# Kernel tuning notes

Measured on AMD Instinct MI355X. Metric: run time of the kernel, lower is better.

The kernel has to match this reference:

```python
import jax, jax.numpy as jnp
import numpy as np

B, S, D = 1, 2048, 2048
H, HKV, HD = 16, 8, 128
WINDOW = 1024
EPS = 1e-6
SCALE = HD ** -0.5


def _rope_tables(seq_len, head_dim, theta=10000.0):
    inv_freq = 1.0 / (theta ** (jnp.arange(0, head_dim, 2, dtype=jnp.float32) / head_dim))
    ang = jnp.arange(seq_len, dtype=jnp.float32)[:, None] * inv_freq[None, :]  # [S, hd/2]
    emb = jnp.concatenate([ang, ang], axis=-1)  # [S, hd]
    return jnp.cos(emb)[None], jnp.sin(emb)[None]  # [1, S, hd]


def setup_inputs() -> dict:
    key = jax.random.key(0)
    ks = jax.random.split(key, 8)
    cos, sin = _rope_tables(S, HD)
    return {
        "hidden_states": jax.random.normal(ks[0], (B, S, D), jnp.float32),
        "cos": jnp.broadcast_to(cos, (B, S, HD)),
        "sin": jnp.broadcast_to(sin, (B, S, HD)),
        "Wq": jax.random.normal(ks[1], (D, H * HD), jnp.float32) * (D ** -0.5),
        "Wk": jax.random.normal(ks[2], (D, HKV * HD), jnp.float32) * (D ** -0.5),
        "Wv": jax.random.normal(ks[3], (D, HKV * HD), jnp.float32) * (D ** -0.5),
        "Wo": jax.random.normal(ks[4], (H * HD, D), jnp.float32) * ((H * HD) ** -0.5),
        "q_scale": jax.random.uniform(ks[5], (HD,), jnp.float32, 0.5, 1.5),
        "k_scale": jax.random.uniform(ks[6], (HD,), jnp.float32, 0.5, 1.5),
    }


def _rms_norm(x, scale):
    # per-head RMSNorm over last dim, computed in fp32 (matches RMSNorm module)
    xf = x.astype(jnp.float32)
    var = jnp.mean(xf * xf, axis=-1, keepdims=True)
    return (xf * jax.lax.rsqrt(var + EPS) * scale).astype(x.dtype)


def _rotate_half(x):
    x1, x2 = x[..., : HD // 2], x[..., HD // 2 :]
    return jnp.concatenate([-x2, x1], axis=-1)


def _apply_rope(x, cos, sin):
    # cos/sin: [B,S,hd] -> [B,S,1,hd] (unsqueeze_dim=2)
    c, s = cos[:, :, None, :], sin[:, :, None, :]
    return x * c + _rotate_half(x) * s


def reference(hidden_states, cos, sin, Wq, Wk, Wv, Wo, q_scale, k_scale):
    b, s, _ = hidden_states.shape
    q = (hidden_states @ Wq).reshape(b, s, H, HD)
    k = (hidden_states @ Wk).reshape(b, s, HKV, HD)
    v = (hidden_states @ Wv).reshape(b, s, HKV, HD)
    q = _rms_norm(q, q_scale)
    k = _rms_norm(k, k_scale)
    q = _apply_rope(q, cos, sin)
    k = _apply_rope(k, cos, sin)
    # GQA: repeat kv heads to match query heads (groups are consecutive)
    g = H // HKV
    k = jnp.repeat(k, g, axis=2)  # [b, s, H, hd]
    v = jnp.repeat(v, g, axis=2)
    scores = jnp.einsum("bqhd,bkhd->bhqk", q, k) * SCALE  # [b,H,S,S]
    i = jnp.arange(s)[:, None]
    j = jnp.arange(s)[None, :]
    allowed = (j <= i) & (i - j <= WINDOW)  # causal + sliding window
    scores = jnp.where(allowed[None, None], scores, -jnp.inf)
    attn = jax.nn.softmax(scores, axis=-1)
    out = jnp.einsum("bhqk,bkhd->bqhd", attn, v).reshape(b, s, H * HD)
    return out @ Wo
```

## Files before the change

kernel.cpp:

```cpp
#include <hip/hip_runtime.h>
#include <hip/hip_bf16.h>
#include <cmath>


typedef __bf16 bf16x8 __attribute__((ext_vector_type(8)));
typedef float  f32x4  __attribute__((ext_vector_type(4)));

#define S_LEN    2048
#define NH       16
#define NKV      8
#define HDIM     128
#define WIN      1024
#define QK_SCALE_L2E 0.12751744595f
#define RMS_EPS  1e-6f

__device__ __forceinline__ void gld16(void* lds, const void* g) {
    __builtin_amdgcn_global_load_lds(
        (const __attribute__((address_space(1))) unsigned int*)g,
        (__attribute__((address_space(3))) unsigned int*)lds, 16, 0, 0);
}

__device__ __forceinline__ unsigned short f2bu(float x) {
    __hip_bfloat16 h = __float2bfloat16(x);
    return *(unsigned short*)&h;
}

__global__ __launch_bounds__(256) void trans_cvt_kernel(
    const float* __restrict__ Wq, const float* __restrict__ Wk,
    const float* __restrict__ Wv, const float* __restrict__ Wo,
    const float* __restrict__ hs,
    __hip_bfloat16* __restrict__ WqkvT, __hip_bfloat16* __restrict__ WoT,
    __hip_bfloat16* __restrict__ hsb)
{
    __shared__ __attribute__((aligned(16))) unsigned short tile[64][72];
    int id = blockIdx.x;
    if (id >= 3072) {
        size_t i = ((size_t)(id - 3072) * 256 + threadIdx.x) * 8;
        float4 a = *(const float4*)(hs + i);
        float4 b = *(const float4*)(hs + i + 4);
        unsigned short u[8] = { f2bu(a.x), f2bu(a.y), f2bu(a.z), f2bu(a.w),
                                f2bu(b.x), f2bu(b.y), f2bu(b.z), f2bu(b.w) };
        *(uint4*)(hsb + i) = *(uint4*)u;
        return;
    }
    const float* src; __hip_bfloat16* dst; int N, kt, nt;
    if (id < 1024)      { src = Wq; dst = WqkvT;                          N = 2048; kt = id >> 5;          nt = id & 31; }
    else if (id < 1536) { src = Wk; dst = WqkvT + (size_t)2048*2048;      N = 1024; kt = (id-1024) >> 4;   nt = (id-1024) & 15; }
    else if (id < 2048) { src = Wv; dst = WqkvT + (size_t)3072*2048;      N = 1024; kt = (id-1536) >> 4;   nt = (id-1536) & 15; }
    else                { src = Wo; dst = WoT;                            N = 2048; kt = (id-2048) >> 5;   nt = (id-2048) & 31; }
    int k0 = kt * 64, n0 = nt * 64;
    int tid = threadIdx.x;
#pragma unroll
    for (int p = 0; p < 2; ++p) {
        int c = p*256 + tid; int r = c >> 3, cc = (c & 7) * 8;
        const float* s = src + (size_t)(k0 + r)*N + n0 + cc;
        float4 a = *(const float4*)s;
        float4 b = *(const float4*)(s + 4);
        unsigned short u[8] = { f2bu(a.x), f2bu(a.y), f2bu(a.z), f2bu(a.w),
                                f2bu(b.x), f2bu(b.y), f2bu(b.z), f2bu(b.w) };
        *(uint4*)&tile[r][cc] = *(uint4*)u;
    }
    __syncthreads();
#pragma unroll
    for (int p = 0; p < 2; ++p) {
        int c = p*256 + tid; int r2 = c >> 3, c2 = (c & 7) * 8;
        uint4 o;
        o.x = tile[c2+0][r2] | ((unsigned)tile[c2+1][r2] << 16);
        o.y = tile[c2+2][r2] | ((unsigned)tile[c2+3][r2] << 16);
        o.z = tile[c2+4][r2] | ((unsigned)tile[c2+5][r2] << 16);
        o.w = tile[c2+6][r2] | ((unsigned)tile[c2+7][r2] << 16);
        *(uint4*)(dst + (size_t)(n0 + r2)*2048 + k0 + c2) = o;
    }
}

template <typename OT>
__global__ __launch_bounds__(256) void gemm_bt_kernel(
    const __hip_bfloat16* __restrict__ A, const __hip_bfloat16* __restrict__ BT,
    OT* __restrict__ C, int M, int N, int K)
{
    __shared__ __attribute__((aligned(16))) __hip_bfloat16 As[128*32];
    __shared__ __attribute__((aligned(16))) __hip_bfloat16 Bs[128*32];
    const int tid  = threadIdx.x;
    const int lane = tid & 63;
    const int wave = tid >> 6;
    const int quad = lane >> 4, l15 = lane & 15;
    const int m0 = blockIdx.y * 128, n0 = blockIdx.x * 128;
    const int wm = (wave >> 1) * 64, wn = (wave & 1) * 64;
    const int sw = (quad ^ ((l15 >> 1) & 3)) * 8;

    f32x4 acc[4][4] = {};

    for (int k0 = 0; k0 < K; k0 += 32) {
#pragma unroll
        for (int p = 0; p < 2; ++p) {
            int c = p*256 + tid;
            int row = c >> 2, seg = c & 3;
            int cs = seg ^ ((row >> 1) & 3);
            gld16((char*)As + c*16, A  + (size_t)(m0 + row)*K + k0 + cs*8);
            gld16((char*)Bs + c*16, BT + (size_t)(n0 + row)*K + k0 + cs*8);
        }
        __syncthreads();
        bf16x8 af[4], bfr[4];
#pragma unroll
        for (int t = 0; t < 4; ++t) {
            af[t]  = *(const bf16x8*)(As + (wm + t*16 + l15)*32 + sw);
            bfr[t] = *(const bf16x8*)(Bs + (wn + t*16 + l15)*32 + sw);
        }
#pragma unroll
        for (int mt = 0; mt < 4; ++mt)
#pragma unroll
            for (int nt = 0; nt < 4; ++nt)
                acc[mt][nt] = __builtin_amdgcn_mfma_f32_16x16x32_bf16(af[mt], bfr[nt], acc[mt][nt], 0, 0, 0);
        __syncthreads();
    }
#pragma unroll
    for (int mt = 0; mt < 4; ++mt)
#pragma unroll
        for (int nt = 0; nt < 4; ++nt)
#pragma unroll
            for (int r = 0; r < 4; ++r) {
                int row = m0 + wm + mt*16 + quad*4 + r;
                int col = n0 + wn + nt*16 + l15;
                if constexpr (__is_same(OT, float))
                    C[(size_t)row*N + col] = acc[mt][nt][r];
                else
                    C[(size_t)row*N + col] = __float2bfloat16(acc[mt][nt][r]);
            }
}

__global__ __launch_bounds__(256) void rms_vt_kernel(
    const __hip_bfloat16* __restrict__ qkv,
    const float* __restrict__ cosb, const float* __restrict__ sinb,
    const float* __restrict__ qsc,  const float* __restrict__ ksc,
    __hip_bfloat16* __restrict__ Qn, __hip_bfloat16* __restrict__ Kn,
    __hip_bfloat16* __restrict__ Vt)
{
    __shared__ __attribute__((aligned(16))) unsigned short tile[64][72];
    int id = blockIdx.x;
    if (id >= 2048) {
        int t  = id - 2048;
        int s0 = (t & 31) * 64;
        int v0 = (t >> 5) * 64;
        int tid = threadIdx.x;
#pragma unroll
        for (int p = 0; p < 2; ++p) {
            int c = p*256 + tid; int r = c >> 3, cc = (c & 7) * 8;
            uint4 v = *(const uint4*)(qkv + (size_t)(s0 + r)*4096 + 3072 + v0 + cc);
            *(uint4*)&tile[r][cc] = v;
        }
        __syncthreads();
#pragma unroll
        for (int p = 0; p < 2; ++p) {
            int c = p*256 + tid; int r2 = c >> 3, c2 = (c & 7) * 8;
            uint4 o;
            o.x = tile[c2+0][r2] | ((unsigned)tile[c2+1][r2] << 16);
            o.y = tile[c2+2][r2] | ((unsigned)tile[c2+3][r2] << 16);
            o.z = tile[c2+4][r2] | ((unsigned)tile[c2+5][r2] << 16);
            o.w = tile[c2+6][r2] | ((unsigned)tile[c2+7][r2] << 16);
            *(uint4*)(Vt + (size_t)(v0 + r2)*2048 + s0 + c2) = o;
        }
        return;
    }
    int s = id;
    int wave = threadIdx.x >> 6, lane = threadIdx.x & 63;
    float c1 = cosb[s*128 + lane];
    float c2 = cosb[s*128 + 64 + lane];
    float s1 = sinb[s*128 + lane];
    float s2 = sinb[s*128 + 64 + lane];
    for (int u = wave; u < 24; u += 4) {
        bool isq = (u < 16);
        int h = isq ? u : u - 16;
        const __hip_bfloat16* x = qkv + (size_t)s*4096 + (isq ? h*128 : 2048 + h*128);
        float x1 = (float)x[lane], x2 = (float)x[lane + 64];
        float ss = x1*x1 + x2*x2;
#pragma unroll
        for (int off = 32; off; off >>= 1) ss += __shfl_xor(ss, off);
        float r = rsqrtf(ss * (1.0f/128.0f) + RMS_EPS);
        if (isq) r *= QK_SCALE_L2E;
        const float* sc = isq ? qsc : ksc;
        float y1 = x1 * r * sc[lane];
        float y2 = x2 * r * sc[lane + 64];
        float o1 = y1*c1 - y2*s1;
        float o2 = y2*c2 + y1*s2;
        __hip_bfloat16* dst = isq ? (Qn + (size_t)s*2048 + h*128)
                                  : (Kn + (size_t)s*1024 + h*128);
        dst[lane]      = __float2bfloat16(o1);
        dst[lane + 64] = __float2bfloat16(o2);
    }
}

__global__ __launch_bounds__(256, 2) void attn_kernel(
    const __hip_bfloat16* __restrict__ Qn,
    const __hip_bfloat16* __restrict__ Kn,
    const __hip_bfloat16* __restrict__ Vt,
    __hip_bfloat16* __restrict__ O)
{
    __shared__ __attribute__((aligned(16))) __hip_bfloat16 Ksm[2][64*128];
    __shared__ __attribute__((aligned(16))) __hip_bfloat16 Vsm[2][128*64];
    __shared__ __attribute__((aligned(16))) __hip_bfloat16 P[4][16][76];

    const int bx   = blockIdx.x;
    const int h    = bx & 15;
    const int qb   = 31 - (bx >> 4);
    const int i0   = qb * 64;
    const int hk   = h >> 1;
    const int tid  = threadIdx.x, wave = tid >> 6, lane = tid & 63;
    const int quad = lane >> 4, l15 = lane & 15;
    const int ib   = i0 + wave * 16;

    const __hip_bfloat16* Kh = Kn + hk * HDIM;
    const __hip_bfloat16* Vh = Vt + (size_t)(hk * HDIM) * 2048;

    bf16x8 qf[4];
    const __hip_bfloat16* qbase = Qn + (size_t)(ib + l15)*2048 + h*HDIM + quad*8;
#pragma unroll
    for (int kk = 0; kk < 4; ++kk) qf[kk] = *(const bf16x8*)(qbase + kk*32);

    f32x4 o[8] = {};
    float lrow[4] = {0.f, 0.f, 0.f, 0.f};

    int j_lo = i0 - WIN; if (j_lo < 0) j_lo = 0;
    const int jstart = j_lo & ~63;
    const int jend   = i0;

    auto stage = [&](int b, int j0) {
#pragma unroll
        for (int p = 0; p < 4; ++p) {
            int L = p*256 + tid;
            int r = L >> 4;
            int c = (L & 15) ^ (r & 15);
            gld16((char*)&Ksm[b][0] + L*16, Kh + (size_t)(j0 + r)*1024 + c*8);
        }
#pragma unroll
        for (int p = 0; p < 4; ++p) {
            int L = p*256 + tid;
            int dv = L >> 3;
            int c = (L & 7) ^ (dv & 7);
            gld16((char*)&Vsm[b][0] + L*16, Vh + (size_t)dv*2048 + j0 + c*8);
        }
    };

    stage(0, jstart);
    int cur = 0;
    for (int j0 = jstart; j0 <= jend; j0 += 64, cur ^= 1) {
        __syncthreads();
        if (j0 + 64 <= jend) stage(cur ^ 1, j0 + 64);

        f32x4 sacc[4] = {};
#pragma unroll
        for (int nt = 0; nt < 4; ++nt) {
            const int r = nt*16 + l15;
#pragma unroll
            for (int kk = 0; kk < 4; ++kk) {
                const int cc = (kk*4 + quad) ^ l15;
                bf16x8 kfr = *(const bf16x8*)(&Ksm[cur][0] + r*128 + cc*8);
                sacc[nt] = __builtin_amdgcn_mfma_f32_16x16x32_bf16(qf[kk], kfr, sacc[nt], 0, 0, 0);
            }
        }

        const bool need_mask = (j0 + 63 > ib) || (j0 < ib + 15 - WIN);
        if (need_mask) {
#pragma unroll
            for (int nt = 0; nt < 4; ++nt) {
                int j = j0 + nt*16 + l15;
#pragma unroll
                for (int r = 0; r < 4; ++r) {
                    int i = ib + quad*4 + r;
                    bool valid = (j <= i) && (i - j <= WIN);
                    float p = valid ? __builtin_exp2f(sacc[nt][r]) : 0.f;
                    lrow[r] += p;
                    P[wave][quad*4 + r][nt*16 + l15] = __float2bfloat16(p);
                }
            }
        } else {
#pragma unroll
            for (int nt = 0; nt < 4; ++nt)
#pragma unroll
                for (int r = 0; r < 4; ++r) {
                    float p = __builtin_exp2f(sacc[nt][r]);
                    lrow[r] += p;
                    P[wave][quad*4 + r][nt*16 + l15] = __float2bfloat16(p);
                }
        }

#pragma unroll
        for (int ks = 0; ks < 2; ++ks) {
            bf16x8 pf = *(const bf16x8*)&P[wave][l15][ks*32 + quad*8];
#pragma unroll
            for (int dt = 0; dt < 8; ++dt) {
                const int dv = dt*16 + l15;
                const int cc = (ks*4 + quad) ^ (l15 & 7);
                bf16x8 vfr = *(const bf16x8*)(&Vsm[cur][0] + dv*64 + cc*8);
                o[dt] = __builtin_amdgcn_mfma_f32_16x16x32_bf16(pf, vfr, o[dt], 0, 0, 0);
            }
        }
    }

#pragma unroll
    for (int r = 0; r < 4; ++r) {
        lrow[r] += __shfl_xor(lrow[r], 1);
        lrow[r] += __shfl_xor(lrow[r], 2);
        lrow[r] += __shfl_xor(lrow[r], 4);
        lrow[r] += __shfl_xor(lrow[r], 8);
        float inv = 1.0f / lrow[r];
        int row = ib + quad*4 + r;
#pragma unroll
        for (int dt = 0; dt < 8; ++dt)
            O[(size_t)row*2048 + h*HDIM + dt*16 + l15] = __float2bfloat16(o[dt][r] * inv);
    }
}

extern "C" void kernel_launch(void* const* d_in, const int* in_sizes, int n_in,
                              void* d_out, int out_size, void* d_ws, size_t ws_size,
                              hipStream_t stream)
{
    (void)in_sizes; (void)n_in; (void)out_size; (void)ws_size;
    const float* hs   = (const float*)d_in[0];
    const float* cosb = (const float*)d_in[1];
    const float* sinb = (const float*)d_in[2];
    const float* Wq   = (const float*)d_in[3];
    const float* Wk   = (const float*)d_in[4];
    const float* Wv   = (const float*)d_in[5];
    const float* Wo   = (const float*)d_in[6];
    const float* qs   = (const float*)d_in[7];
    const float* ks   = (const float*)d_in[8];

    char* ws = (char*)d_ws;
    __hip_bfloat16* WqkvT = (__hip_bfloat16*)(ws);
    __hip_bfloat16* WoT   = (__hip_bfloat16*)(ws + (16u << 20));
    __hip_bfloat16* QKV   = (__hip_bfloat16*)(ws + (24u << 20));
    __hip_bfloat16* Qn    = (__hip_bfloat16*)(ws + (40u << 20));
    __hip_bfloat16* Kn    = (__hip_bfloat16*)(ws + (48u << 20));
    __hip_bfloat16* Vt    = (__hip_bfloat16*)(ws + (52u << 20));
    __hip_bfloat16* hsb   = (__hip_bfloat16*)(ws + (56u << 20));
    __hip_bfloat16* AT    = (__hip_bfloat16*)(ws + (56u << 20));

    trans_cvt_kernel<<<dim3(5120), dim3(256), 0, stream>>>(Wq, Wk, Wv, Wo, hs, WqkvT, WoT, hsb);
    gemm_bt_kernel<__hip_bfloat16><<<dim3(32, 16), dim3(256), 0, stream>>>(hsb, WqkvT, QKV, 2048, 4096, 2048);
    rms_vt_kernel<<<dim3(2560), dim3(256), 0, stream>>>(QKV, cosb, sinb, qs, ks, Qn, Kn, Vt);
    attn_kernel<<<dim3(512), dim3(256), 0, stream>>>(Qn, Kn, Vt, AT);
    gemm_bt_kernel<float><<<dim3(16, 16), dim3(256), 0, stream>>>(AT, WoT, (float*)d_out, 2048, 2048, 2048);
}
```

Measured before the change: 254.1 us.

## Double-buffer GEMM LDS tiles with BK=64 and XOR-8 swizzle

```diff
diff --git a/kernel.cpp b/kernel.cpp
--- a/kernel.cpp
+++ b/kernel.cpp
@@ -74,44 +74,60 @@
 }
 
 template <typename OT>
-__global__ __launch_bounds__(256) void gemm_bt_kernel(
+__global__ __launch_bounds__(256, 2) void gemm_bt_kernel(
     const __hip_bfloat16* __restrict__ A, const __hip_bfloat16* __restrict__ BT,
     OT* __restrict__ C, int M, int N, int K)
 {
-    __shared__ __attribute__((aligned(16))) __hip_bfloat16 As[128*32];
-    __shared__ __attribute__((aligned(16))) __hip_bfloat16 Bs[128*32];
+    __shared__ __attribute__((aligned(16))) __hip_bfloat16 As[2][128*64];
+    __shared__ __attribute__((aligned(16))) __hip_bfloat16 Bs[2][128*64];
     const int tid  = threadIdx.x;
     const int lane = tid & 63;
     const int wave = tid >> 6;
     const int quad = lane >> 4, l15 = lane & 15;
     const int m0 = blockIdx.y * 128, n0 = blockIdx.x * 128;
     const int wm = (wave >> 1) * 64, wn = (wave & 1) * 64;
-    const int sw = (quad ^ ((l15 >> 1) & 3)) * 8;
+    const int sw = l15 & 7;
 
     f32x4 acc[4][4] = {};
 
-    for (int k0 = 0; k0 < K; k0 += 32) {
-#pragma unroll
-        for (int p = 0; p < 2; ++p) {
-            int c = p*256 + tid;
-            int row = c >> 2, seg = c & 3;
-            int cs = seg ^ ((row >> 1) & 3);
-            gld16((char*)As + c*16, A  + (size_t)(m0 + row)*K + k0 + cs*8);
-            gld16((char*)Bs + c*16, BT + (size_t)(n0 + row)*K + k0 + cs*8);
-        }
+    auto stage = [&](int b, int k0) {
+#pragma unroll
+        for (int p = 0; p < 4; ++p) {
+            int L = p*256 + tid;
+            int r = L >> 3, s = L & 7;
+            int cs = s ^ (r & 7);
+            gld16((char*)&As[b][0] + L*16, A + (size_t)(m0 + r)*K + k0 + cs*8);
+        }
+#pragma unroll
+        for (int p = 0; p < 4; ++p) {
+            int L = p*256 + tid;
+            int r = L >> 3, s = L & 7;
+            int cs = s ^ (r & 7);
+            gld16((char*)&Bs[b][0] + L*16, BT + (size_t)(n0 + r)*K + k0 + cs*8);
+        }
+    };
+
+    const int NT = K >> 6;
+    stage(0, 0);
+    int cur = 0;
+    for (int kt = 0; kt < NT; ++kt, cur ^= 1) {
         __syncthreads();
-        bf16x8 af[4], bfr[4];
-#pragma unroll
-        for (int t = 0; t < 4; ++t) {
-            af[t]  = *(const bf16x8*)(As + (wm + t*16 + l15)*32 + sw);
-            bfr[t] = *(const bf16x8*)(Bs + (wn + t*16 + l15)*32 + sw);
-        }
-#pragma unroll
-        for (int mt = 0; mt < 4; ++mt)
-#pragma unroll
-            for (int nt = 0; nt < 4; ++nt)
-                acc[mt][nt] = __builtin_amdgcn_mfma_f32_16x16x32_bf16(af[mt], bfr[nt], acc[mt][nt], 0, 0, 0);
-        __syncthreads();
+        if (kt + 1 < NT) stage(cur ^ 1, (kt + 1) << 6);
+#pragma unroll
+        for (int ks = 0; ks < 2; ++ks) {
+            const int slot = ((ks*4 + quad) ^ sw) * 8;
+            bf16x8 af[4], bfr[4];
+#pragma unroll
+            for (int t = 0; t < 4; ++t) {
+                af[t]  = *(const bf16x8*)(&As[cur][0] + (wm + t*16 + l15)*64 + slot);
+                bfr[t] = *(const bf16x8*)(&Bs[cur][0] + (wn + t*16 + l15)*64 + slot);
+            }
+#pragma unroll
+            for (int mt = 0; mt < 4; ++mt)
+#pragma unroll
+                for (int nt = 0; nt < 4; ++nt)
+                    acc[mt][nt] = __builtin_amdgcn_mfma_f32_16x16x32_bf16(af[mt], bfr[nt], acc[mt][nt], 0, 0, 0);
+        }
     }
 #pragma unroll
     for (int mt = 0; mt < 4; ++mt)
```

Result: faster. 230.2 us (-9.4%).
